# Kernel optimization log

Hardware: AMD Instinct MI355X
Metric: run time of the kernel (lower is better)

The kernel has to match this reference:

```python
import jax, jax.numpy as jnp
import numpy as np

H = 1024  # HIDDEN_LAYER_SIZE

def _xavier(key, shape, gain=0.01):
    fan_out, fan_in = shape
    a = gain * np.sqrt(6.0 / (fan_in + fan_out))
    return jax.random.uniform(key, shape, jnp.float32, -a, a)

def setup_inputs() -> dict:
    key = jax.random.key(0)
    ks = jax.random.split(key, 7)
    B = 65536
    white_features = jax.random.uniform(ks[0], (B, 768), jnp.float32)
    black_features = jax.random.uniform(ks[1], (B, 768), jnp.float32)
    stm = jax.random.uniform(ks[2], (B, 1), jnp.float32)
    return {
        "white_features": white_features,
        "black_features": black_features,
        "stm": stm,
        "ft_w": _xavier(ks[3], (H, 768)),
        "ft_b": jnp.zeros((H,), jnp.float32),
        "l1_w": _xavier(ks[4], (8, 2 * H)),
        "l1_b": jnp.zeros((8,), jnp.float32),
        "l2_w": _xavier(ks[5], (32, 8)),
        "l2_b": jnp.zeros((32,), jnp.float32),
        "l3_w": _xavier(ks[6], (1, 32)),
        "l3_b": jnp.zeros((1,), jnp.float32),
    }

def reference(white_features, black_features, stm, ft_w, ft_b,
              l1_w, l1_b, l2_w, l2_b, l3_w, l3_b):
    w = white_features @ ft_w.T + ft_b  # [B, H]
    b = black_features @ ft_w.T + ft_b  # [B, H]
    acc = stm * jnp.concatenate([w, b], axis=1) + (1.0 - stm) * jnp.concatenate([b, w], axis=1)
    l1_x = jnp.clip(acc, 0.0, 1.0)
    l2_x = jnp.clip(l1_x @ l1_w.T + l1_b, 0.0, 1.0)
    l3_x = jnp.clip(l2_x @ l2_w.T + l2_b, 0.0, 1.0)
    raw_output = l3_x @ l3_w.T + l3_b  # [B, 1]
    output = jax.nn.sigmoid(raw_output)
    return (output, raw_output)
```

## Files before the change

### kernel.cpp

```cpp
#include <hip/hip_runtime.h>
#include <cmath>

typedef float f4_t __attribute__((ext_vector_type(4)));

#define B_TOTAL   65536
#define FTW_SCALE 1024.0f
#define INV_SCALE (1.0f/1024.0f)

__global__ void pack_ftw_kernel(const float* __restrict__ ftw, char* __restrict__ ws)
{
    int t   = blockIdx.x * 256 + threadIdx.x;
    int nl  = t & 15;
    int q   = (t >> 4) & 3;
    int cfg = (t >> 6) & 7;
    int tk  = t >> 9;
    int kk  = tk % 24;
    int nc  = tk / 24;
    int row = nc * 128 + cfg * 16 + nl;
    int k0  = kk * 32 + q * 8;
    const float* src = ftw + (size_t)row * 768 + k0;
    float4 x = *(const float4*)(src);
    float4 y = *(const float4*)(src + 4);
    int v0 = __builtin_amdgcn_cvt_pk_fp8_f32(x.x * FTW_SCALE, x.y * FTW_SCALE, 0, false);
    v0     = __builtin_amdgcn_cvt_pk_fp8_f32(x.z * FTW_SCALE, x.w * FTW_SCALE, v0, true);
    int v1 = __builtin_amdgcn_cvt_pk_fp8_f32(y.x * FTW_SCALE, y.y * FTW_SCALE, 0, false);
    v1     = __builtin_amdgcn_cvt_pk_fp8_f32(y.z * FTW_SCALE, y.w * FTW_SCALE, v1, true);
    int2 o; o.x = v0; o.y = v1;
    *(int2*)(ws + (size_t)t * 8) = o;
}

__global__ __launch_bounds__(256, 3) void nnue_fused_kernel(
    const float* __restrict__ wf,  const float* __restrict__ bfeat,
    const float* __restrict__ stm, const char*  __restrict__ ftw8,
    const float* __restrict__ ftb, const float* __restrict__ l1w,
    const float* __restrict__ l1b, const float* __restrict__ l2w,
    const float* __restrict__ l2b, const float* __restrict__ l3w,
    const float* __restrict__ l3b, float* __restrict__ out)
{
    __shared__ char  Atile[64 * 784];
    __shared__ float l1acc[2][32][8];

    const int t    = threadIdx.x;
    const int lane = t & 63;
    const int wave = t >> 6;
    const int wm   = wave >> 1;
    const int wn   = wave & 1;
    const int q    = lane >> 4;
    const int nl   = lane & 15;
    const int s0   = blockIdx.x * 32;

    {
        const int row = t >> 3;
        const int c8  = t & 7;
        const float4* wsrc = (const float4*)(wf    + (size_t)(s0 + row) * 768);
        const float4* bsrc = (const float4*)(bfeat + (size_t)(s0 + row) * 768);
        char* dw = &Atile[row * 784];
        char* db = &Atile[(row + 32) * 784];
        #pragma unroll
        for (int it = 0; it < 24; ++it) {
            int f4i = c8 + it * 8;
            float4 x = wsrc[f4i];
            int v = __builtin_amdgcn_cvt_pk_fp8_f32(x.x, x.y, 0, false);
            v     = __builtin_amdgcn_cvt_pk_fp8_f32(x.z, x.w, v, true);
            *(int*)(dw + f4i * 4) = v;
            float4 y = bsrc[f4i];
            int u = __builtin_amdgcn_cvt_pk_fp8_f32(y.x, y.y, 0, false);
            u     = __builtin_amdgcn_cvt_pk_fp8_f32(y.z, y.w, u, true);
            *(int*)(db + f4i * 4) = u;
        }
    }

    float sreg[4];
    #pragma unroll
    for (int r = 0; r < 4; ++r) sreg[r] = stm[s0 + wm * 16 + q * 4 + r];

    __syncthreads();

    float p[4][8];
    #pragma unroll
    for (int r = 0; r < 4; ++r)
        #pragma unroll
        for (int o = 0; o < 8; ++o) p[r][o] = 0.f;

    const char* bbase = ftw8 + wn * 2048 + (size_t)lane * 8;
    const char* arW   = &Atile[(wm * 16 + nl) * 784 + q * 8];
    const char* arB   = arW + 32 * 784;

    for (int nc = 0; nc < 8; ++nc) {
        f4_t aw[4], ab[4];
        #pragma unroll
        for (int cf = 0; cf < 4; ++cf) {
            aw[cf] = (f4_t){0.f, 0.f, 0.f, 0.f};
            ab[cf] = (f4_t){0.f, 0.f, 0.f, 0.f};
        }
        const char* bnc = bbase + (size_t)nc * 24 * 4096;

        #pragma unroll 2
        for (int kk = 0; kk < 24; ++kk) {
            long a0 = *(const long*)(arW + kk * 32);
            long a1 = *(const long*)(arB + kk * 32);
            const char* bt = bnc + kk * 4096;
            long b0 = *(const long*)(bt);
            long b1 = *(const long*)(bt + 512);
            long b2 = *(const long*)(bt + 1024);
            long b3 = *(const long*)(bt + 1536);
            aw[0] = __builtin_amdgcn_mfma_f32_16x16x32_fp8_fp8(a0, b0, aw[0], 0, 0, 0);
            ab[0] = __builtin_amdgcn_mfma_f32_16x16x32_fp8_fp8(a1, b0, ab[0], 0, 0, 0);
            aw[1] = __builtin_amdgcn_mfma_f32_16x16x32_fp8_fp8(a0, b1, aw[1], 0, 0, 0);
            ab[1] = __builtin_amdgcn_mfma_f32_16x16x32_fp8_fp8(a1, b1, ab[1], 0, 0, 0);
            aw[2] = __builtin_amdgcn_mfma_f32_16x16x32_fp8_fp8(a0, b2, aw[2], 0, 0, 0);
            ab[2] = __builtin_amdgcn_mfma_f32_16x16x32_fp8_fp8(a1, b2, ab[2], 0, 0, 0);
            aw[3] = __builtin_amdgcn_mfma_f32_16x16x32_fp8_fp8(a0, b3, aw[3], 0, 0, 0);
            ab[3] = __builtin_amdgcn_mfma_f32_16x16x32_fp8_fp8(a1, b3, ab[3], 0, 0, 0);
        }

        #pragma unroll
        for (int cf = 0; cf < 4; ++cf) {
            int j = nc * 128 + wn * 64 + cf * 16 + nl;
            float bias = ftb[j];
            float lo[8], hi[8];
            #pragma unroll
            for (int o = 0; o < 8; ++o) {
                lo[o] = l1w[o * 2048 + j];
                hi[o] = l1w[o * 2048 + 1024 + j];
            }
            #pragma unroll
            for (int r = 0; r < 4; ++r) {
                float wv = fmaf(aw[cf][r], INV_SCALE, bias);
                float bv = fmaf(ab[cf][r], INV_SCALE, bias);
                float d  = wv - bv;
                float first  = fmaf(sreg[r], d, bv);
                float second = fmaf(-sreg[r], d, wv);
                first  = fminf(fmaxf(first,  0.f), 1.f);
                second = fminf(fmaxf(second, 0.f), 1.f);
                #pragma unroll
                for (int o = 0; o < 8; ++o)
                    p[r][o] = fmaf(first, lo[o], fmaf(second, hi[o], p[r][o]));
            }
        }
    }

    #pragma unroll
    for (int m = 1; m < 16; m <<= 1)
        #pragma unroll
        for (int r = 0; r < 4; ++r)
            #pragma unroll
            for (int o = 0; o < 8; ++o)
                p[r][o] += __shfl_xor(p[r][o], m);

    if (nl == 0) {
        #pragma unroll
        for (int r = 0; r < 4; ++r)
            #pragma unroll
            for (int o = 0; o < 8; ++o)
                l1acc[wn][wm * 16 + q * 4 + r][o] = p[r][o];
    }
    __syncthreads();

    if (t < 32) {
        float v[8];
        #pragma unroll
        for (int o = 0; o < 8; ++o)
            v[o] = fminf(fmaxf(l1acc[0][t][o] + l1acc[1][t][o] + l1b[o], 0.f), 1.f);
        float raw = l3b[0];
        #pragma unroll
        for (int u = 0; u < 32; ++u) {
            float h = l2b[u];
            #pragma unroll
            for (int o = 0; o < 8; ++o) h = fmaf(v[o], l2w[u * 8 + o], h);
            h = fminf(fmaxf(h, 0.f), 1.f);
            raw = fmaf(h, l3w[u], raw);
        }
        out[s0 + t]           = 1.0f / (1.0f + expf(-raw));
        out[B_TOTAL + s0 + t] = raw;
    }
}

extern "C" void kernel_launch(void* const* d_in, const int* in_sizes, int n_in,
                              void* d_out, int out_size, void* d_ws, size_t ws_size,
                              hipStream_t stream)
{
    const float* wf  = (const float*)d_in[0];
    const float* bf  = (const float*)d_in[1];
    const float* stm = (const float*)d_in[2];
    const float* ftw = (const float*)d_in[3];
    const float* ftb = (const float*)d_in[4];
    const float* l1w = (const float*)d_in[5];
    const float* l1b = (const float*)d_in[6];
    const float* l2w = (const float*)d_in[7];
    const float* l2b = (const float*)d_in[8];
    const float* l3w = (const float*)d_in[9];
    const float* l3b = (const float*)d_in[10];
    char* ws8 = (char*)d_ws;

    hipLaunchKernelGGL(pack_ftw_kernel, dim3(384), dim3(256), 0, stream, ftw, ws8);
    hipLaunchKernelGGL(nnue_fused_kernel, dim3(2048), dim3(256), 0, stream,
                       wf, bf, stm, ws8, ftb, l1w, l1b, l2w, l2b, l3w, l3b,
                       (float*)d_out);
}
```

Measured before the change: 620.5 us.

## Repartition FT GEMM so each wave covers all rows and a disjoint column slice

Switches the fused kernel's wave decomposition from a 2x2 grid to one where each wave takes all 32 samples (both 16-row halves) and its own 256 hidden columns. Each B fragment load now feeds four MFMAs instead of two. B tiles are repacked into 16-byte fragments and the next k-step is prefetched in registers. The A tile is staged into an MFMA-fragment-ordered LDS layout so each lane reads 16 bytes per step, and the float-to-fp8 conversion is restructured to match. The cost is doubled per-thread accumulator and partial-sum register state, which may strain occupancy under launch_bounds(256,3).

```diff
diff --git a/kernel.cpp b/kernel.cpp
--- a/kernel.cpp
+++ b/kernel.cpp
@@ -2,31 +2,38 @@
 #include <cmath>
 
 typedef float f4_t __attribute__((ext_vector_type(4)));
+typedef long  l2_t __attribute__((ext_vector_type(2)));
 
 #define B_TOTAL   65536
 #define FTW_SCALE 1024.0f
 #define INV_SCALE (1.0f/1024.0f)
 
+__device__ __forceinline__ int pk8(float a, float b, float c, float d) {
+    int v = __builtin_amdgcn_cvt_pk_fp8_f32(a, b, 0, false);
+    return  __builtin_amdgcn_cvt_pk_fp8_f32(c, d, v, true);
+}
+__device__ __forceinline__ float clip01(float x) { return fminf(fmaxf(x, 0.f), 1.f); }
+
 __global__ void pack_ftw_kernel(const float* __restrict__ ftw, char* __restrict__ ws)
 {
-    int t   = blockIdx.x * 256 + threadIdx.x;
-    int nl  = t & 15;
-    int q   = (t >> 4) & 3;
-    int cfg = (t >> 6) & 7;
-    int tk  = t >> 9;
-    int kk  = tk % 24;
-    int nc  = tk / 24;
-    int row = nc * 128 + cfg * 16 + nl;
-    int k0  = kk * 32 + q * 8;
-    const float* src = ftw + (size_t)row * 768 + k0;
-    float4 x = *(const float4*)(src);
-    float4 y = *(const float4*)(src + 4);
-    int v0 = __builtin_amdgcn_cvt_pk_fp8_f32(x.x * FTW_SCALE, x.y * FTW_SCALE, 0, false);
-    v0     = __builtin_amdgcn_cvt_pk_fp8_f32(x.z * FTW_SCALE, x.w * FTW_SCALE, v0, true);
-    int v1 = __builtin_amdgcn_cvt_pk_fp8_f32(y.x * FTW_SCALE, y.y * FTW_SCALE, 0, false);
-    v1     = __builtin_amdgcn_cvt_pk_fp8_f32(y.z * FTW_SCALE, y.w * FTW_SCALE, v1, true);
-    int2 o; o.x = v0; o.y = v1;
-    *(int2*)(ws + (size_t)t * 8) = o;
+    int t    = blockIdx.x * 256 + threadIdx.x;
+    int lane = t & 63;
+    int ncp  = (t >> 6) & 31;
+    int kk   = t >> 11;
+    int nl = lane & 15, q = (lane >> 4) & 3;
+    int k0 = kk * 32 + q * 8;
+    const float* p0 = ftw + (size_t)(ncp * 32 + nl) * 768 + k0;
+    const float* p1 = p0 + 16 * 768;
+    float4 x0 = *(const float4*)p0;
+    float4 x1 = *(const float4*)(p0 + 4);
+    float4 y0 = *(const float4*)p1;
+    float4 y1 = *(const float4*)(p1 + 4);
+    int4 o;
+    o.x = pk8(x0.x*FTW_SCALE, x0.y*FTW_SCALE, x0.z*FTW_SCALE, x0.w*FTW_SCALE);
+    o.y = pk8(x1.x*FTW_SCALE, x1.y*FTW_SCALE, x1.z*FTW_SCALE, x1.w*FTW_SCALE);
+    o.z = pk8(y0.x*FTW_SCALE, y0.y*FTW_SCALE, y0.z*FTW_SCALE, y0.w*FTW_SCALE);
+    o.w = pk8(y1.x*FTW_SCALE, y1.y*FTW_SCALE, y1.z*FTW_SCALE, y1.w*FTW_SCALE);
+    *(int4*)(ws + (size_t)t * 16) = o;
 }
 
 __global__ __launch_bounds__(256, 3) void nnue_fused_kernel(
@@ -37,123 +44,155 @@
     const float* __restrict__ l2b, const float* __restrict__ l3w,
     const float* __restrict__ l3b, float* __restrict__ out)
 {
-    __shared__ char  Atile[64 * 784];
-    __shared__ float l1acc[2][32][8];
+    __shared__ char  Ald[24 * 2048];
+    __shared__ float l1part[4][32][8];
 
     const int t    = threadIdx.x;
     const int lane = t & 63;
     const int wave = t >> 6;
-    const int wm   = wave >> 1;
-    const int wn   = wave & 1;
-    const int q    = lane >> 4;
     const int nl   = lane & 15;
+    const int q    = (lane >> 4) & 3;
     const int s0   = blockIdx.x * 32;
 
     {
-        const int row = t >> 3;
-        const int c8  = t & 7;
-        const float4* wsrc = (const float4*)(wf    + (size_t)(s0 + row) * 768);
-        const float4* bsrc = (const float4*)(bfeat + (size_t)(s0 + row) * 768);
-        char* dw = &Atile[row * 784];
-        char* db = &Atile[(row + 32) * 784];
-        #pragma unroll
-        for (int it = 0; it < 24; ++it) {
-            int f4i = c8 + it * 8;
-            float4 x = wsrc[f4i];
-            int v = __builtin_amdgcn_cvt_pk_fp8_f32(x.x, x.y, 0, false);
-            v     = __builtin_amdgcn_cvt_pk_fp8_f32(x.z, x.w, v, true);
-            *(int*)(dw + f4i * 4) = v;
-            float4 y = bsrc[f4i];
-            int u = __builtin_amdgcn_cvt_pk_fp8_f32(y.x, y.y, 0, false);
-            u     = __builtin_amdgcn_cvt_pk_fp8_f32(y.z, y.w, u, true);
-            *(int*)(db + f4i * 4) = u;
-        }
-    }
-
-    float sreg[4];
+        const int kpar = t >> 7;
+        const int tt   = t & 127;
+        const int p    = tt >> 6;
+        const int sl   = tt & 63;
+        const int snl  = sl & 15, sq = (sl >> 4) & 3;
+        const float* base = p ? bfeat : wf;
+        const float* r0 = base + (size_t)(s0 + snl) * 768;
+        const float* r1 = r0 + 16 * 768;
+        char* dst = &Ald[p * 1024 + sl * 16];
+        #pragma unroll 4
+        for (int pass = 0; pass < 12; ++pass) {
+            int kk = pass * 2 + kpar;
+            int k0 = kk * 32 + sq * 8;
+            float4 x0 = *(const float4*)(r0 + k0);
+            float4 x1 = *(const float4*)(r0 + k0 + 4);
+            float4 y0 = *(const float4*)(r1 + k0);
+            float4 y1 = *(const float4*)(r1 + k0 + 4);
+            int4 o;
+            o.x = pk8(x0.x, x0.y, x0.z, x0.w);
+            o.y = pk8(x1.x, x1.y, x1.z, x1.w);
+            o.z = pk8(y0.x, y0.y, y0.z, y0.w);
+            o.w = pk8(y1.x, y1.y, y1.z, y1.w);
+            *(int4*)(dst + kk * 2048) = o;
+        }
+    }
+
+    float s_lo[4], s_hi[4];
     #pragma unroll
-    for (int r = 0; r < 4; ++r) sreg[r] = stm[s0 + wm * 16 + q * 4 + r];
+    for (int r = 0; r < 4; ++r) {
+        s_lo[r] = stm[s0 + q * 4 + r];
+        s_hi[r] = stm[s0 + 16 + q * 4 + r];
+    }
 
     __syncthreads();
 
-    float p[4][8];
+    float pacc[2][4][8];
     #pragma unroll
-    for (int r = 0; r < 4; ++r)
-        #pragma unroll
-        for (int o = 0; o < 8; ++o) p[r][o] = 0.f;
-
-    const char* bbase = ftw8 + wn * 2048 + (size_t)lane * 8;
-    const char* arW   = &Atile[(wm * 16 + nl) * 784 + q * 8];
-    const char* arB   = arW + 32 * 784;
-
-    for (int nc = 0; nc < 8; ++nc) {
-        f4_t aw[4], ab[4];
-        #pragma unroll
-        for (int cf = 0; cf < 4; ++cf) {
-            aw[cf] = (f4_t){0.f, 0.f, 0.f, 0.f};
-            ab[cf] = (f4_t){0.f, 0.f, 0.f, 0.f};
-        }
-        const char* bnc = bbase + (size_t)nc * 24 * 4096;
+    for (int mh = 0; mh < 2; ++mh)
+        #pragma unroll
+        for (int r = 0; r < 4; ++r)
+            #pragma unroll
+            for (int o = 0; o < 8; ++o) pacc[mh][r][o] = 0.f;
+
+    const char* ap = &Ald[lane * 16];
+
+    #pragma unroll 1
+    for (int ng = 0; ng < 4; ++ng) {
+        f4_t aW0[4], aW1[4], aB0[4], aB1[4];
+        #pragma unroll
+        for (int nb = 0; nb < 4; ++nb) {
+            aW0[nb] = (f4_t){0.f,0.f,0.f,0.f};
+            aW1[nb] = (f4_t){0.f,0.f,0.f,0.f};
+            aB0[nb] = (f4_t){0.f,0.f,0.f,0.f};
+            aB1[nb] = (f4_t){0.f,0.f,0.f,0.f};
+        }
+        const char* bp = ftw8 + (size_t)(wave * 8 + ng * 2) * 1024 + lane * 16;
+        l2_t bc0 = *(const l2_t*)(bp);
+        l2_t bc1 = *(const l2_t*)(bp + 1024);
 
         #pragma unroll 2
         for (int kk = 0; kk < 24; ++kk) {
-            long a0 = *(const long*)(arW + kk * 32);
-            long a1 = *(const long*)(arB + kk * 32);
-            const char* bt = bnc + kk * 4096;
-            long b0 = *(const long*)(bt);
-            long b1 = *(const long*)(bt + 512);
-            long b2 = *(const long*)(bt + 1024);
-            long b3 = *(const long*)(bt + 1536);
-            aw[0] = __builtin_amdgcn_mfma_f32_16x16x32_fp8_fp8(a0, b0, aw[0], 0, 0, 0);
-            ab[0] = __builtin_amdgcn_mfma_f32_16x16x32_fp8_fp8(a1, b0, ab[0], 0, 0, 0);
-            aw[1] = __builtin_amdgcn_mfma_f32_16x16x32_fp8_fp8(a0, b1, aw[1], 0, 0, 0);
-            ab[1] = __builtin_amdgcn_mfma_f32_16x16x32_fp8_fp8(a1, b1, ab[1], 0, 0, 0);
-            aw[2] = __builtin_amdgcn_mfma_f32_16x16x32_fp8_fp8(a0, b2, aw[2], 0, 0, 0);
-            ab[2] = __builtin_amdgcn_mfma_f32_16x16x32_fp8_fp8(a1, b2, ab[2], 0, 0, 0);
-            aw[3] = __builtin_amdgcn_mfma_f32_16x16x32_fp8_fp8(a0, b3, aw[3], 0, 0, 0);
-            ab[3] = __builtin_amdgcn_mfma_f32_16x16x32_fp8_fp8(a1, b3, ab[3], 0, 0, 0);
-        }
-
-        #pragma unroll
-        for (int cf = 0; cf < 4; ++cf) {
-            int j = nc * 128 + wn * 64 + cf * 16 + nl;
-            float bias = ftb[j];
+            l2_t bn0, bn1;
+            if (kk < 23) {
+                bn0 = *(const l2_t*)(bp + (size_t)(kk + 1) * 32768);
+                bn1 = *(const l2_t*)(bp + (size_t)(kk + 1) * 32768 + 1024);
+            }
+            l2_t aw = *(const l2_t*)(ap + kk * 2048);
+            l2_t ab = *(const l2_t*)(ap + kk * 2048 + 1024);
+
+            aW0[0] = __builtin_amdgcn_mfma_f32_16x16x32_fp8_fp8(aw.x, bc0.x, aW0[0], 0,0,0);
+            aW1[0] = __builtin_amdgcn_mfma_f32_16x16x32_fp8_fp8(aw.y, bc0.x, aW1[0], 0,0,0);
+            aB0[0] = __builtin_amdgcn_mfma_f32_16x16x32_fp8_fp8(ab.x, bc0.x, aB0[0], 0,0,0);
+            aB1[0] = __builtin_amdgcn_mfma_f32_16x16x32_fp8_fp8(ab.y, bc0.x, aB1[0], 0,0,0);
+            aW0[1] = __builtin_amdgcn_mfma_f32_16x16x32_fp8_fp8(aw.x, bc0.y, aW0[1], 0,0,0);
+            aW1[1] = __builtin_amdgcn_mfma_f32_16x16x32_fp8_fp8(aw.y, bc0.y, aW1[1], 0,0,0);
+            aB0[1] = __builtin_amdgcn_mfma_f32_16x16x32_fp8_fp8(ab.x, bc0.y, aB0[1], 0,0,0);
+            aB1[1] = __builtin_amdgcn_mfma_f32_16x16x32_fp8_fp8(ab.y, bc0.y, aB1[1], 0,0,0);
+            aW0[2] = __builtin_amdgcn_mfma_f32_16x16x32_fp8_fp8(aw.x, bc1.x, aW0[2], 0,0,0);
+            aW1[2] = __builtin_amdgcn_mfma_f32_16x16x32_fp8_fp8(aw.y, bc1.x, aW1[2], 0,0,0);
+            aB0[2] = __builtin_amdgcn_mfma_f32_16x16x32_fp8_fp8(ab.x, bc1.x, aB0[2], 0,0,0);
+            aB1[2] = __builtin_amdgcn_mfma_f32_16x16x32_fp8_fp8(ab.y, bc1.x, aB1[2], 0,0,0);
+            aW0[3] = __builtin_amdgcn_mfma_f32_16x16x32_fp8_fp8(aw.x, bc1.y, aW0[3], 0,0,0);
+            aW1[3] = __builtin_amdgcn_mfma_f32_16x16x32_fp8_fp8(aw.y, bc1.y, aW1[3], 0,0,0);
+            aB0[3] = __builtin_amdgcn_mfma_f32_16x16x32_fp8_fp8(ab.x, bc1.y, aB0[3], 0,0,0);
+            aB1[3] = __builtin_amdgcn_mfma_f32_16x16x32_fp8_fp8(ab.y, bc1.y, aB1[3], 0,0,0);
+
+            if (kk < 23) { bc0 = bn0; bc1 = bn1; }
+        }
+
+        #pragma unroll
+        for (int nb = 0; nb < 4; ++nb) {
+            int col = wave * 256 + ng * 64 + nb * 16 + nl;
+            float bias = ftb[col];
+            const float* l1c = l1w + col;
             float lo[8], hi[8];
             #pragma unroll
             for (int o = 0; o < 8; ++o) {
-                lo[o] = l1w[o * 2048 + j];
-                hi[o] = l1w[o * 2048 + 1024 + j];
+                lo[o] = l1c[o * 2048];
+                hi[o] = l1c[o * 2048 + 1024];
             }
             #pragma unroll
             for (int r = 0; r < 4; ++r) {
-                float wv = fmaf(aw[cf][r], INV_SCALE, bias);
-                float bv = fmaf(ab[cf][r], INV_SCALE, bias);
-                float d  = wv - bv;
-                float first  = fmaf(sreg[r], d, bv);
-                float second = fmaf(-sreg[r], d, wv);
-                first  = fminf(fmaxf(first,  0.f), 1.f);
-                second = fminf(fmaxf(second, 0.f), 1.f);
+                float w0 = fmaf(aW0[nb][r], INV_SCALE, bias);
+                float b0 = fmaf(aB0[nb][r], INV_SCALE, bias);
+                float w1 = fmaf(aW1[nb][r], INV_SCALE, bias);
+                float b1 = fmaf(aB1[nb][r], INV_SCALE, bias);
+                float d0 = w0 - b0, d1 = w1 - b1;
+                float f0 = clip01(fmaf( s_lo[r], d0, b0));
+                float g0 = clip01(fmaf(-s_lo[r], d0, w0));
+                float f1 = clip01(fmaf( s_hi[r], d1, b1));
+                float g1 = clip01(fmaf(-s_hi[r], d1, w1));
+                #pragma unroll
+                for (int o = 0; o < 8; ++o) {
+                    pacc[0][r][o] = fmaf(f0, lo[o], fmaf(g0, hi[o], pacc[0][r][o]));
+                    pacc[1][r][o] = fmaf(f1, lo[o], fmaf(g1, hi[o], pacc[1][r][o]));
+                }
+            }
+        }
+    }
+
+    #pragma unroll
+    for (int m = 1; m < 16; m <<= 1)
+        #pragma unroll
+        for (int mh = 0; mh < 2; ++mh)
+            #pragma unroll
+            for (int r = 0; r < 4; ++r)
                 #pragma unroll
                 for (int o = 0; o < 8; ++o)
-                    p[r][o] = fmaf(first, lo[o], fmaf(second, hi[o], p[r][o]));
-            }
-        }
-    }
-
-    #pragma unroll
-    for (int m = 1; m < 16; m <<= 1)
-        #pragma unroll
-        for (int r = 0; r < 4; ++r)
-            #pragma unroll
-            for (int o = 0; o < 8; ++o)
-                p[r][o] += __shfl_xor(p[r][o], m);
+                    pacc[mh][r][o] += __shfl_xor(pacc[mh][r][o], m);
 
     if (nl == 0) {
         #pragma unroll
-        for (int r = 0; r < 4; ++r)
-            #pragma unroll
-            for (int o = 0; o < 8; ++o)
-                l1acc[wn][wm * 16 + q * 4 + r][o] = p[r][o];
+        for (int mh = 0; mh < 2; ++mh)
+            #pragma unroll
+            for (int r = 0; r < 4; ++r)
+                #pragma unroll
+                for (int o = 0; o < 8; ++o)
+                    l1part[wave][mh * 16 + q * 4 + r][o] = pacc[mh][r][o];
     }
     __syncthreads();
 
@@ -161,14 +200,15 @@
         float v[8];
         #pragma unroll
         for (int o = 0; o < 8; ++o)
-            v[o] = fminf(fmaxf(l1acc[0][t][o] + l1acc[1][t][o] + l1b[o], 0.f), 1.f);
+            v[o] = clip01(l1part[0][t][o] + l1part[1][t][o] +
+                          l1part[2][t][o] + l1part[3][t][o] + l1b[o]);
         float raw = l3b[0];
         #pragma unroll
         for (int u = 0; u < 32; ++u) {
             float h = l2b[u];
             #pragma unroll
             for (int o = 0; o < 8; ++o) h = fmaf(v[o], l2w[u * 8 + o], h);
-            h = fminf(fmaxf(h, 0.f), 1.f);
+            h = clip01(h);
             raw = fmaf(h, l3w[u], raw);
         }
         out[s0 + t]           = 1.0f / (1.0f + expf(-raw));
@@ -193,7 +233,7 @@
     const float* l3b = (const float*)d_in[10];
     char* ws8 = (char*)d_ws;
 
-    hipLaunchKernelGGL(pack_ftw_kernel, dim3(384), dim3(256), 0, stream, ftw, ws8);
+    hipLaunchKernelGGL(pack_ftw_kernel, dim3(192), dim3(256), 0, stream, ftw, ws8);
     hipLaunchKernelGGL(nnue_fused_kernel, dim3(2048), dim3(256), 0, stream,
                        wf, bf, stm, ws8, ftb, l1w, l1b, l2w, l2b, l3w, l3b,
                        (float*)d_out);
```

After: 636.5 us. 2.6% more time.
